# Optimization experiments

Hardware: AMD Instinct MI355X
Metric: run time of the kernel (lower is better)

## Reference

```python
import jax, jax.numpy as jnp
import numpy as np
from jax import lax

M, G = 16, 4
INP = 256
OUP = 256
K = 3
EPS = 1e-5


def _weightnet(x, gap_vec, fc1_w, fc1_b, fc2_w, inp, oup, stride):
    # x: [B, inp, H, W], gap_vec: [B, 16]
    B, _, H, W = x.shape
    a = jax.nn.sigmoid(gap_vec @ fc1_w.T + fc1_b)          # [B, M*oup]
    groups = G * oup                                        # 1024
    out_pg = (oup * inp * K * K) // groups                  # 576
    in_pg = (M * oup) // groups                             # 4
    a = a.reshape(B, groups, in_pg)
    w2 = fc2_w.reshape(groups, out_pg, in_pg)
    # grouped 1x1 conv generating per-sample conv weights
    xw = jnp.einsum('bgi,goi->bgo', a, w2)                  # [B, groups, out_pg]
    xw = xw.reshape(B * oup, inp, K, K)                     # per-sample kernels
    xr = x.reshape(1, B * inp, H, W)
    out = lax.conv_general_dilated(
        xr, xw, (stride, stride), [(1, 1), (1, 1)],
        dimension_numbers=('NCHW', 'OIHW', 'NCHW'),
        feature_group_count=B)
    return out.reshape(B, oup, out.shape[2], out.shape[3])


def _bn(x, g, b, m, v):
    scale = (g / jnp.sqrt(v + EPS))[:, None, None]
    return (x - m[:, None, None]) * scale + b[:, None, None]


def setup_inputs() -> dict:
    key = jax.random.key(0)
    ks = jax.random.split(key, 20)
    d = {}
    d['x'] = jax.random.normal(ks[0], (32, 256, 56, 56), jnp.float32)
    d['reduce_w'] = jax.random.normal(ks[1], (16, 256), jnp.float32) * 0.05
    d['reduce_b'] = jax.random.normal(ks[2], (16,), jnp.float32) * 0.05
    d['w1_fc1_w'] = jax.random.normal(ks[3], (4096, 16), jnp.float32) * 0.05
    d['w1_fc1_b'] = jax.random.normal(ks[4], (4096,), jnp.float32) * 0.05
    d['w1_fc2_w'] = jax.random.normal(ks[5], (589824, 4), jnp.float32) * 0.05
    d['bn1_g'] = jax.random.uniform(ks[6], (256,), jnp.float32) + 0.5
    d['bn1_b'] = jax.random.normal(ks[7], (256,), jnp.float32) * 0.05
    d['bn1_m'] = jax.random.normal(ks[8], (256,), jnp.float32) * 0.05
    d['bn1_v'] = jax.random.uniform(ks[9], (256,), jnp.float32) + 0.5
    d['w2_fc1_w'] = jax.random.normal(ks[10], (4096, 16), jnp.float32) * 0.05
    d['w2_fc1_b'] = jax.random.normal(ks[11], (4096,), jnp.float32) * 0.05
    d['w2_fc2_w'] = jax.random.normal(ks[12], (589824, 4), jnp.float32) * 0.05
    d['bn2_g'] = jax.random.uniform(ks[13], (256,), jnp.float32) + 0.5
    d['bn2_b'] = jax.random.normal(ks[14], (256,), jnp.float32) * 0.05
    d['bn2_m'] = jax.random.normal(ks[15], (256,), jnp.float32) * 0.05
    d['bn2_v'] = jax.random.uniform(ks[16], (256,), jnp.float32) + 0.5
    return d


def reference(x, reduce_w, reduce_b, w1_fc1_w, w1_fc1_b, w1_fc2_w,
              bn1_g, bn1_b, bn1_m, bn1_v,
              w2_fc1_w, w2_fc1_b, w2_fc2_w,
              bn2_g, bn2_b, bn2_m, bn2_v):
    # global average pool -> reduce 1x1 conv
    gap = x.mean(axis=(2, 3))                       # [B, in_planes]
    gap = gap @ reduce_w.T + reduce_b               # [B, 16]
    out = _weightnet(x, gap, w1_fc1_w, w1_fc1_b, w1_fc2_w, INP, OUP, 1)
    out = jax.nn.relu(_bn(out, bn1_g, bn1_b, bn1_m, bn1_v))
    out = _weightnet(out, gap, w2_fc1_w, w2_fc1_b, w2_fc2_w, OUP, OUP, 1)
    out = _bn(out, bn2_g, bn2_b, bn2_m, bn2_v)
    out = out + x                                   # identity shortcut (stride=1, in==out)
    return jax.nn.relu(out)
```

## Files before the change

### kernel.cpp

```cpp
#include <hip/hip_runtime.h>

typedef short bf16x8 __attribute__((ext_vector_type(8)));
typedef float f32x4 __attribute__((ext_vector_type(4)));

#define EPSV 1e-5f
#define BNUM 32
#define CH 256
#define HW 3136
#define PXT 3684
#define NCHUNK 32
#define PERB_SHORTS (NCHUNK*PXT*8)
#define WB_PERB 589824

__device__ __forceinline__ unsigned short f2bf(float f) {
  unsigned int u = __float_as_uint(f);
  u += 0x7fffu + ((u >> 16) & 1u);
  return (unsigned short)(u >> 16);
}

__device__ __forceinline__ void gld16(const void* g, void* l) {
  __builtin_amdgcn_global_load_lds((const __attribute__((address_space(1))) void*)g,
                                   (__attribute__((address_space(3))) void*)l,
                                   16, 0, 0);
}

__global__ void k_gap16(const float* __restrict__ gapc, const float* __restrict__ rw,
                        const float* __restrict__ rb, float* __restrict__ g16) {
  int b = blockIdx.x;
  int t = threadIdx.x;
  int j = t >> 5;
  int c0 = t & 31;
  const float* gc = gapc + b * 256;
  const float* w = rw + j * 256;
  float s = 0.f;
#pragma unroll
  for (int k = 0; k < 8; ++k) s += gc[c0 + k * 32] * w[c0 + k * 32];
  for (int off = 16; off; off >>= 1) s += __shfl_down(s, off, 32);
  if (c0 == 0) g16[b * 16 + j] = s * (1.f / 3136.f) + rb[j];
}

__global__ void k_act(const float* __restrict__ g16,
                      const float* __restrict__ w1w, const float* __restrict__ w1b,
                      const float* __restrict__ w2w, const float* __restrict__ w2b,
                      float* __restrict__ a1, float* __restrict__ a2) {
  int idx = blockIdx.x * 256 + threadIdx.x;
  int which = idx >> 17;
  int r = idx & 131071;
  int b = r >> 12, m = r & 4095;
  const float* w = (which ? w2w : w1w) + m * 16;
  float s = which ? w2b[m] : w1b[m];
  const float* g = g16 + b * 16;
#pragma unroll
  for (int j = 0; j < 16; ++j) s += g[j] * w[j];
  float out = 1.f / (1.f + __expf(-s));
  (which ? a2 : a1)[r] = out;
}

__global__ void k_zero(unsigned short* __restrict__ xp1, unsigned short* __restrict__ xp2) {
  int bc = blockIdx.x;
  int t = threadIdx.x;
  uint4 z = {0u, 0u, 0u, 0u};
  for (int wbuf = 0; wbuf < 2; ++wbuf) {
    unsigned short* base = (wbuf ? xp2 : xp1) + (size_t)bc * (PXT * 8);
    uint4* p = (uint4*)base;
    if (t < 123) p[t] = z;
    p[3370 + t] = z;
    if (t < 58) p[3626 + t] = z;
    if (t < 56) {
      int e = 64 + (t + 1) * 58 + 57;
      p[e] = z;
      p[e + 1] = z;
    }
  }
}

__global__ void k_xpad(const float* __restrict__ x, unsigned short* __restrict__ xp,
                       float* __restrict__ gapc) {
  int y = blockIdx.x, ch = blockIdx.y, b = blockIdx.z;
  int l = threadIdx.x;
  bool act = (l < 56);
  int lc = act ? l : 0;
  const float* src = x + ((size_t)(b * 256 + ch * 8)) * HW + y * 56 + lc;
  float v[8];
#pragma unroll
  for (int k = 0; k < 8; ++k) v[k] = act ? src[k * HW] : 0.f;
  if (act) {
    ushort4 lo, hi;
    lo.x = f2bf(v[0]); lo.y = f2bf(v[1]); lo.z = f2bf(v[2]); lo.w = f2bf(v[3]);
    hi.x = f2bf(v[4]); hi.y = f2bf(v[5]); hi.z = f2bf(v[6]); hi.w = f2bf(v[7]);
    unsigned short* dst = xp + ((size_t)(b * NCHUNK + ch)) * (PXT * 8)
                             + (size_t)(64 + (y + 1) * 58 + (l + 1)) * 8;
    *(ushort4*)dst = lo;
    *(ushort4*)(dst + 4) = hi;
  }
#pragma unroll
  for (int k = 0; k < 8; ++k) {
    float s = v[k];
    for (int off = 32; off; off >>= 1) s += __shfl_down(s, off, 64);
    if (l == 0) atomicAdd(&gapc[b * 256 + ch * 8 + k], s);
  }
}

__global__ void k_wgen(const float* __restrict__ a, const float4* __restrict__ w2,
                       unsigned short* __restrict__ wb) {
  int og = blockIdx.x & 63, bg = blockIdx.x >> 6;
  int t = threadIdx.x;
  for (int it = 0; it < 36; ++it) {
    int wi = it * 256 + t;
    int oc_l = wi / 2304;
    int r = wi - oc_l * 2304;
    int ic = r / 9;
    int k9 = r - ic * 9;
    int kh = k9 / 3;
    int kw = k9 - kh * 3;
    int oc = og * 4 + oc_l;
    int g = oc * 4 + (ic >> 6);
    int o = (ic & 63) * 9 + k9;
    float4 w4 = w2[g * 576 + o];
    int s_ = ic >> 5, kc_ = (ic >> 3) & 3, icl = ic & 7;
    int ocg_ = oc >> 7, ocl_ = oc & 127;
    size_t off = (size_t)((kh * 8 + s_) * 2 + ocg_) * 12288 + kc_ * 3072 + ocl_ * 24
               + kw * 8 + icl;
#pragma unroll
    for (int bi = 0; bi < 4; ++bi) {
      int b = bg * 4 + bi;
      float4 a4 = *(const float4*)(a + b * 4096 + g * 4);
      float s = w4.x * a4.x + w4.y * a4.y + w4.z * a4.z + w4.w * a4.w;
      wb[(size_t)b * WB_PERB + off] = f2bf(s);
    }
  }
}

__global__ __launch_bounds__(256, 2)
void k_conv(const unsigned short* __restrict__ xpad,
            const unsigned short* __restrict__ wbuf,
            const float* __restrict__ bgp, const float* __restrict__ bbp,
            const float* __restrict__ bmp, const float* __restrict__ bvp,
            const float* __restrict__ resid,
            unsigned short* __restrict__ outpad,
            float* __restrict__ outf,
            const int mode) {
  __shared__ unsigned short sW[2][12288];
  __shared__ unsigned short sX[12288];

  const int tid = threadIdx.x;
  const int lane = tid & 63;
  const int wv = tid >> 6;
  const int wocg = wv >> 1;
  const int wpxg = wv & 1;
  const int ocl = lane & 15;
  const int kc = lane >> 4;

  int rid = blockIdx.x;
  int xcd = rid & 7;
  int j = rid >> 3;
  int b = xcd + 8 * (j / 30);
  int slot = j % 30;
  int bocg = slot & 1;
  int p0 = 58 + (slot >> 1) * 224;

  const unsigned short* xb = xpad + (size_t)b * PERB_SHORTS + 64 * 8;
  const unsigned short* wbb = wbuf + (size_t)b * WB_PERB + bocg * 12288;

  f32x4 acc[4][7];
#pragma unroll
  for (int i = 0; i < 4; ++i)
#pragma unroll
    for (int k = 0; k < 7; ++k)
      acc[i][k] = (f32x4){0.f, 0.f, 0.f, 0.f};

  auto STAGE_W = [&](int t, int buf) {
    int s = t / 3;
    int kh = t - s * 3;
    const unsigned short* wsrc = wbb + (size_t)(kh * 8 + s) * 24576;
#pragma unroll
    for (int i = 0; i < 6; ++i) {
      int seg = wv * 6 + i;
      gld16(wsrc + seg * 512 + lane * 8, &sW[buf][seg * 512]);
    }
  };
  auto STAGE_X = [&](int s) {
    const unsigned short* xs = xb + ((long)(s * 4 + wv) * PXT + p0 - 59) * 8;
#pragma unroll
    for (int i = 0; i < 6; ++i)
      gld16(xs + (i * 64 + lane) * 8, &sX[wv * 3072 + i * 512]);
  };

  STAGE_X(0);
  STAGE_W(0, 0);
  int cur = 0;
  for (int s8 = 0; s8 < 8; ++s8) {
    asm volatile("s_waitcnt vmcnt(0)" ::: "memory");
    __builtin_amdgcn_s_barrier();
#pragma unroll
    for (int kh = 0; kh < 3; ++kh) {
      int t = s8 * 3 + kh;
      if (t + 1 < 24) {
        STAGE_W(t + 1, cur ^ 1);
        asm volatile("s_waitcnt vmcnt(6)" ::: "memory");
      } else {
        asm volatile("s_waitcnt vmcnt(0)" ::: "memory");
      }
      __builtin_amdgcn_s_barrier();
#pragma unroll
      for (int kw = 0; kw < 3; ++kw) {
        bf16x8 af[4], bfr[7];
#pragma unroll
        for (int fm = 0; fm < 4; ++fm)
          af[fm] = *(const bf16x8*)&sW[cur][kc * 3072 + (wocg * 64 + fm * 16 + ocl) * 24 + kw * 8];
#pragma unroll
        for (int fn = 0; fn < 7; ++fn)
          bfr[fn] = *(const bf16x8*)&sX[kc * 3072 + (kh * 58 + wpxg * 112 + fn * 16 + ocl + kw) * 8];
        __builtin_amdgcn_s_setprio(1);
#pragma unroll
        for (int fm = 0; fm < 4; ++fm)
#pragma unroll
          for (int fn = 0; fn < 7; ++fn)
            acc[fm][fn] = __builtin_amdgcn_mfma_f32_16x16x32_bf16(af[fm], bfr[fn], acc[fm][fn], 0, 0, 0);
        __builtin_amdgcn_s_setprio(0);
      }
      __builtin_amdgcn_s_barrier();
      if (kh == 2 && s8 + 1 < 8) STAGE_X(s8 + 1);
      cur ^= 1;
    }
  }

  float* scb = (float*)&sX[0];
  if (tid < 128) {
    int oc = bocg * 128 + tid;
    float sc = bgp[oc] * rsqrtf(bvp[oc] + EPSV);
    scb[tid] = sc;
    scb[128 + tid] = bbp[oc] - bmp[oc] * sc;
  }
  __syncthreads();

  const int dpb = wpxg * 112 + ocl;
  if (mode == 1) {
#pragma unroll
    for (int fn = 0; fn < 7; ++fn) {
      int pp = p0 + dpb + fn * 16;
      int py = pp / 58;
      int px = pp - py * 58;
      if (py < 1 || py > 56 || px < 1 || px > 56) continue;
#pragma unroll
      for (int fm = 0; fm < 4; ++fm) {
        int loc = wocg * 64 + fm * 16 + kc * 4;
        f32x4 v = acc[fm][fn];
        ushort4 w;
        w.x = f2bf(fmaxf(v[0] * scb[loc + 0] + scb[128 + loc + 0], 0.f));
        w.y = f2bf(fmaxf(v[1] * scb[loc + 1] + scb[128 + loc + 1], 0.f));
        w.z = f2bf(fmaxf(v[2] * scb[loc + 2] + scb[128 + loc + 2], 0.f));
        w.w = f2bf(fmaxf(v[3] * scb[loc + 3] + scb[128 + loc + 3], 0.f));
        int ocg_g = bocg * 128 + loc;
        *(ushort4*)&outpad[((size_t)(b * NCHUNK + (ocg_g >> 3))) * (PXT * 8)
                           + (size_t)(64 + pp) * 8 + (ocg_g & 7)] = w;
      }
    }
  } else {
#pragma unroll
    for (int fn = 0; fn < 7; ++fn) {
      int pp = p0 + dpb + fn * 16;
      int py = pp / 58;
      int px = pp - py * 58;
      if (py < 1 || py > 56 || px < 1 || px > 56) continue;
      int obase = (py - 1) * 56 + (px - 1);
#pragma unroll
      for (int fm = 0; fm < 4; ++fm) {
        int loc = wocg * 64 + fm * 16 + kc * 4;
        f32x4 v = acc[fm][fn];
#pragma unroll
        for (int r = 0; r < 4; ++r) {
          int oc = bocg * 128 + loc + r;
          size_t oi = ((size_t)(b * CH + oc)) * HW + obase;
          float tv = v[r] * scb[loc + r] + scb[128 + loc + r] + resid[oi];
          outf[oi] = fmaxf(tv, 0.f);
        }
      }
    }
  }
}

#define OFF_XP1 ((size_t)0)
#define XP_BYTES ((size_t)BNUM * PERB_SHORTS * 2)
#define OFF_XP2 (OFF_XP1 + XP_BYTES)
#define OFF_WB  (OFF_XP2 + XP_BYTES)
#define WB_BYTES ((size_t)BNUM * WB_PERB * 2)
#define OFF_GAPC (OFF_WB + WB_BYTES)
#define OFF_G16  (OFF_GAPC + 32768)
#define OFF_A1   (OFF_G16 + 2048)
#define OFF_A2   (OFF_A1 + 524288)

extern "C" void kernel_launch(void* const* d_in, const int* in_sizes, int n_in,
                              void* d_out, int out_size, void* d_ws, size_t ws_size,
                              hipStream_t stream) {
  (void)in_sizes; (void)n_in; (void)out_size; (void)ws_size;
  const float* x        = (const float*)d_in[0];
  const float* reduce_w = (const float*)d_in[1];
  const float* reduce_b = (const float*)d_in[2];
  const float* w1fc1w   = (const float*)d_in[3];
  const float* w1fc1b   = (const float*)d_in[4];
  const float* w1fc2w   = (const float*)d_in[5];
  const float* bn1g     = (const float*)d_in[6];
  const float* bn1b     = (const float*)d_in[7];
  const float* bn1m     = (const float*)d_in[8];
  const float* bn1v     = (const float*)d_in[9];
  const float* w2fc1w   = (const float*)d_in[10];
  const float* w2fc1b   = (const float*)d_in[11];
  const float* w2fc2w   = (const float*)d_in[12];
  const float* bn2g     = (const float*)d_in[13];
  const float* bn2b     = (const float*)d_in[14];
  const float* bn2m     = (const float*)d_in[15];
  const float* bn2v     = (const float*)d_in[16];

  char* ws = (char*)d_ws;
  unsigned short* xp1 = (unsigned short*)(ws + OFF_XP1);
  unsigned short* xp2 = (unsigned short*)(ws + OFF_XP2);
  unsigned short* wb  = (unsigned short*)(ws + OFF_WB);
  float* gapc = (float*)(ws + OFF_GAPC);
  float* g16  = (float*)(ws + OFF_G16);
  float* a1   = (float*)(ws + OFF_A1);
  float* a2   = (float*)(ws + OFF_A2);
  float* outf = (float*)d_out;

  hipMemsetAsync(gapc, 0, 32 * 256 * 4, stream);
  k_zero<<<1024, 256, 0, stream>>>(xp1, xp2);
  k_xpad<<<dim3(56, NCHUNK, BNUM), 64, 0, stream>>>(x, xp1, gapc);
  k_gap16<<<BNUM, 512, 0, stream>>>(gapc, reduce_w, reduce_b, g16);
  k_act<<<1024, 256, 0, stream>>>(g16, w1fc1w, w1fc1b, w2fc1w, w2fc1b, a1, a2);

  k_wgen<<<512, 256, 0, stream>>>(a1, (const float4*)w1fc2w, wb);
  k_conv<<<960, 256, 0, stream>>>(xp1, wb, bn1g, bn1b, bn1m, bn1v,
                                  nullptr, xp2, nullptr, 1);
  k_wgen<<<512, 256, 0, stream>>>(a2, (const float4*)w2fc2w, wb);
  k_conv<<<960, 256, 0, stream>>>(xp2, wb, bn2g, bn2b, bn2m, bn2v,
                                  x, nullptr, outf, 2);
}
```

Baseline: 472.0 us.

## Replace GAP atomics with deterministic partials; restructure conv LDS barriers

k_xpad now handles four rows per 256-thread block and writes per-block partial channel sums to a buffer, replacing global atomicAdd and the memset. k_gap16 then reduces those partials in shared memory. In the conv main loop, the per-stage wait and barrier move out of the loop. An explicit lgkmcnt wait and a sched_barrier go before the MFMA block, a barrier follows each kw step, and X staging moves after the kh loop. These changes aim to cut atomic contention, launch overhead and stalls, at the cost of more barriers per stage.

Result: faster. 395.8 us (-16.1%).

```diff
diff --git a/kernel.cpp b/kernel.cpp
--- a/kernel.cpp
+++ b/kernel.cpp
@@ -24,17 +24,25 @@
                                    16, 0, 0);
 }
 
-__global__ void k_gap16(const float* __restrict__ gapc, const float* __restrict__ rw,
+__global__ void k_gap16(const float* __restrict__ part, const float* __restrict__ rw,
                         const float* __restrict__ rb, float* __restrict__ g16) {
+  __shared__ float gcs[256];
   int b = blockIdx.x;
   int t = threadIdx.x;
+  if (t < 256) {
+    const float* p = part + ((size_t)(b * 32 + (t >> 3)) * 8 + (t & 7)) * 16;
+    float s = 0.f;
+#pragma unroll
+    for (int i = 0; i < 14; ++i) s += p[i];
+    gcs[t] = s;
+  }
+  __syncthreads();
   int j = t >> 5;
   int c0 = t & 31;
-  const float* gc = gapc + b * 256;
   const float* w = rw + j * 256;
   float s = 0.f;
 #pragma unroll
-  for (int k = 0; k < 8; ++k) s += gc[c0 + k * 32] * w[c0 + k * 32];
+  for (int k = 0; k < 8; ++k) s += gcs[c0 + k * 32] * w[c0 + k * 32];
   for (int off = 16; off; off >>= 1) s += __shfl_down(s, off, 32);
   if (c0 == 0) g16[b * 16 + j] = s * (1.f / 3136.f) + rb[j];
 }
@@ -75,9 +83,11 @@
 }
 
 __global__ void k_xpad(const float* __restrict__ x, unsigned short* __restrict__ xp,
-                       float* __restrict__ gapc) {
-  int y = blockIdx.x, ch = blockIdx.y, b = blockIdx.z;
-  int l = threadIdx.x;
+                       float* __restrict__ part) {
+  int y4 = blockIdx.x, ch = blockIdx.y, b = blockIdx.z;
+  int t = threadIdx.x;
+  int r = t >> 6, l = t & 63;
+  int y = y4 * 4 + r;
   bool act = (l < 56);
   int lc = act ? l : 0;
   const float* src = x + ((size_t)(b * 256 + ch * 8)) * HW + y * 56 + lc;
@@ -93,12 +103,17 @@
     *(ushort4*)dst = lo;
     *(ushort4*)(dst + 4) = hi;
   }
+  __shared__ float red[4][8];
 #pragma unroll
   for (int k = 0; k < 8; ++k) {
     float s = v[k];
     for (int off = 32; off; off >>= 1) s += __shfl_down(s, off, 64);
-    if (l == 0) atomicAdd(&gapc[b * 256 + ch * 8 + k], s);
-  }
+    if (l == 0) red[r][k] = s;
+  }
+  __syncthreads();
+  if (t < 8)
+    part[((size_t)(b * 32 + ch) * 8 + t) * 16 + y4]
+        = red[0][t] + red[1][t] + red[2][t] + red[3][t];
 }
 
 __global__ void k_wgen(const float* __restrict__ a, const float4* __restrict__ w2,
@@ -188,10 +203,11 @@
 
   STAGE_X(0);
   STAGE_W(0, 0);
+  asm volatile("s_waitcnt vmcnt(0)" ::: "memory");
+  __builtin_amdgcn_s_barrier();
+
   int cur = 0;
   for (int s8 = 0; s8 < 8; ++s8) {
-    asm volatile("s_waitcnt vmcnt(0)" ::: "memory");
-    __builtin_amdgcn_s_barrier();
 #pragma unroll
     for (int kh = 0; kh < 3; ++kh) {
       int t = s8 * 3 + kh;
@@ -211,6 +227,8 @@
 #pragma unroll
         for (int fn = 0; fn < 7; ++fn)
           bfr[fn] = *(const bf16x8*)&sX[kc * 3072 + (kh * 58 + wpxg * 112 + fn * 16 + ocl + kw) * 8];
+        asm volatile("s_waitcnt lgkmcnt(0)" ::: "memory");
+        __builtin_amdgcn_sched_barrier(0);
         __builtin_amdgcn_s_setprio(1);
 #pragma unroll
         for (int fm = 0; fm < 4; ++fm)
@@ -218,11 +236,11 @@
           for (int fn = 0; fn < 7; ++fn)
             acc[fm][fn] = __builtin_amdgcn_mfma_f32_16x16x32_bf16(af[fm], bfr[fn], acc[fm][fn], 0, 0, 0);
         __builtin_amdgcn_s_setprio(0);
+        __builtin_amdgcn_s_barrier();
       }
-      __builtin_amdgcn_s_barrier();
-      if (kh == 2 && s8 + 1 < 8) STAGE_X(s8 + 1);
       cur ^= 1;
     }
+    if (s8 + 1 < 8) STAGE_X(s8 + 1);
   }
 
   float* scb = (float*)&sX[0];
@@ -285,8 +303,8 @@
 #define OFF_XP2 (OFF_XP1 + XP_BYTES)
 #define OFF_WB  (OFF_XP2 + XP_BYTES)
 #define WB_BYTES ((size_t)BNUM * WB_PERB * 2)
-#define OFF_GAPC (OFF_WB + WB_BYTES)
-#define OFF_G16  (OFF_GAPC + 32768)
+#define OFF_PART (OFF_WB + WB_BYTES)
+#define OFF_G16  (OFF_PART + 262144)
 #define OFF_A1   (OFF_G16 + 2048)
 #define OFF_A2   (OFF_A1 + 524288)
 
@@ -316,16 +334,15 @@
   unsigned short* xp1 = (unsigned short*)(ws + OFF_XP1);
   unsigned short* xp2 = (unsigned short*)(ws + OFF_XP2);
   unsigned short* wb  = (unsigned short*)(ws + OFF_WB);
-  float* gapc = (float*)(ws + OFF_GAPC);
+  float* part = (float*)(ws + OFF_PART);
   float* g16  = (float*)(ws + OFF_G16);
   float* a1   = (float*)(ws + OFF_A1);
   float* a2   = (float*)(ws + OFF_A2);
   float* outf = (float*)d_out;
 
-  hipMemsetAsync(gapc, 0, 32 * 256 * 4, stream);
   k_zero<<<1024, 256, 0, stream>>>(xp1, xp2);
-  k_xpad<<<dim3(56, NCHUNK, BNUM), 64, 0, stream>>>(x, xp1, gapc);
-  k_gap16<<<BNUM, 512, 0, stream>>>(gapc, reduce_w, reduce_b, g16);
+  k_xpad<<<dim3(14, NCHUNK, BNUM), 256, 0, stream>>>(x, xp1, part);
+  k_gap16<<<BNUM, 512, 0, stream>>>(part, reduce_w, reduce_b, g16);
   k_act<<<1024, 256, 0, stream>>>(g16, w1fc1w, w1fc1b, w2fc1w, w2fc1b, a1, a2);
 
   k_wgen<<<512, 256, 0, stream>>>(a1, (const float4*)w1fc2w, wb);
```
